# Performance work log

Measured on AMD Instinct MI355X. Metric: run time of the kernel, lower is better.

Reference implementation:

```python
import jax, jax.numpy as jnp
import numpy as np

N_IN, N_OUT, KNN, N_EL = 100000, 25000, 9, 200000
B, C_IN, C_OUT = 4, 8, 16


def setup_inputs() -> dict:
    key = jax.random.key(0)
    ks = jax.random.split(key, 16)
    M = N_OUT * KNN
    inp = {
        "features": jax.random.normal(ks[0], (B, C_IN, N_IN), jnp.float32),
        "domain_points": jax.random.uniform(ks[1], (N_IN, 2), jnp.float32),
        "range_points": jax.random.uniform(ks[2], (N_OUT, 2), jnp.float32),
        # kNN structure: each range point i has exactly KNN support edges
        "eval_idx_dst": jnp.repeat(jnp.arange(N_OUT, dtype=jnp.int32), KNN),
        "eval_idx_src": jax.random.randint(ks[3], (M,), 0, N_IN, jnp.int32),
        "element_list": jax.random.randint(ks[4], (N_EL, 3), 0, N_IN, jnp.int32),
        # Siren filter MLP: 2 -> 16 x5 -> C_IN*C_OUT (outermost linear)
        "siren_w_in": jax.random.normal(ks[5], (2, 16), jnp.float32) / jnp.sqrt(2.0),
        "siren_b_in": jax.random.normal(ks[6], (16,), jnp.float32) * 0.1,
        "siren_wh": jax.random.normal(ks[7], (4, 16, 16), jnp.float32) / 4.0,
        "siren_bh": jax.random.normal(ks[8], (4, 16), jnp.float32) * 0.1,
        "siren_w_out": jax.random.normal(ks[9], (16, C_IN * C_OUT), jnp.float32) / 4.0,
        "siren_b_out": jax.random.normal(ks[10], (C_IN * C_OUT,), jnp.float32) * 0.1,
        # weight_map: 6 -> 8 -> 8 -> 8 -> 3, all sigmoid
        "wm_w0": jax.random.normal(ks[11], (6, 8), jnp.float32) / jnp.sqrt(6.0),
        "wm_b0": jnp.zeros((8,), jnp.float32),
        "wm_w1": jax.random.normal(ks[12], (8, 8), jnp.float32) / jnp.sqrt(8.0),
        "wm_b1": jnp.zeros((8,), jnp.float32),
        "wm_w2": jax.random.normal(ks[13], (8, 8), jnp.float32) / jnp.sqrt(8.0),
        "wm_b2": jnp.zeros((8,), jnp.float32),
        "wm_w3": jax.random.normal(ks[14], (8, 3), jnp.float32) / jnp.sqrt(8.0),
        "wm_b3": jnp.zeros((3,), jnp.float32),
    }
    return inp


def reference(features, domain_points, range_points, eval_idx_src, eval_idx_dst,
              element_list, siren_w_in, siren_b_in, siren_wh, siren_bh,
              siren_w_out, siren_b_out, wm_w0, wm_b0, wm_w1, wm_b1,
              wm_w2, wm_b2, wm_w3, wm_b3):
    omega_0 = 1.0
    n_in = domain_points.shape[0]
    n_out = range_points.shape[0]
    c_in = features.shape[1]
    c_out = siren_w_out.shape[1] // c_in

    # --- eval_weight_map: per-element MLP + scatter_add to per-node weights ---
    el_pts = domain_points[element_list].reshape(element_list.shape[0], -1)  # [E, 6]
    h = jax.nn.sigmoid(el_pts @ wm_w0 + wm_b0)
    h = jax.nn.sigmoid(h @ wm_w1 + wm_b1)
    h = jax.nn.sigmoid(h @ wm_w2 + wm_b2)
    el_w = jax.nn.sigmoid(h @ wm_w3 + wm_b3)  # [E, 3]
    node_w = jax.ops.segment_sum(el_w.reshape(-1), element_list.reshape(-1),
                                 num_segments=n_in)  # [N_in]
    w = node_w[eval_idx_src]  # [M]

    # --- per-edge Siren filter on relative locations ---
    locs = range_points[eval_idx_dst] - domain_points[eval_idx_src]  # [M, 2]
    h = jnp.sin(omega_0 * (locs @ siren_w_in + siren_b_in))
    for i in range(siren_wh.shape[0]):  # fixed small layer count
        h = jnp.sin(omega_0 * (h @ siren_wh[i] + siren_bh[i]))
    filt = ((h @ siren_w_out + siren_b_out)
            .reshape(-1, c_in, c_out)) / c_in  # [M, C_in, C_out]

    # --- weighted gather -> contract -> scatter (quadrature integral) ---
    gathered = features[:, :, eval_idx_src]  # [B, C_in, M]
    values = jnp.einsum('n,nij,bin->bjn', w, filt, gathered)  # [B, C_out, M]
    seg = jax.ops.segment_sum(values.transpose(2, 0, 1), eval_idx_dst,
                              num_segments=n_out)  # [N_out, B, C_out]
    return seg.transpose(1, 2, 0)  # [B, C_out, N_out]
```

## Files before the change

### kernel.cpp

```cpp
#include <hip/hip_runtime.h>

#define N_IN   100000
#define N_OUT  25000
#define KNN    9
#define N_EL   200000
#define BB     4
#define C_IN   8
#define C_OUT  16
#define M_EDGE (N_OUT * KNN)

#define DPB  28
#define EPB  (DPB * KNN)
#define SOP  65

__global__ void __launch_bounds__(256) elem_kernel(
    const int*   __restrict__ el,
    const float* __restrict__ dp,
    const float* __restrict__ w0, const float* __restrict__ b0,
    const float* __restrict__ w1, const float* __restrict__ b1,
    const float* __restrict__ w2, const float* __restrict__ b2,
    const float* __restrict__ w3, const float* __restrict__ b3,
    float* __restrict__ node_w)
{
    int e = blockIdx.x * 256 + threadIdx.x;
    if (e >= N_EL) return;
    int i0 = el[e*3+0], i1 = el[e*3+1], i2 = el[e*3+2];
    float2 p0 = ((const float2*)dp)[i0];
    float2 p1 = ((const float2*)dp)[i1];
    float2 p2 = ((const float2*)dp)[i2];
    float p[6] = { p0.x, p0.y, p1.x, p1.y, p2.x, p2.y };

    float h[8], h2[8];
#pragma unroll
    for (int k = 0; k < 8; ++k) {
        float t = b0[k];
#pragma unroll
        for (int j = 0; j < 6; ++j) t = fmaf(p[j], w0[j*8+k], t);
        h[k] = 1.f / (1.f + __expf(-t));
    }
#pragma unroll
    for (int k = 0; k < 8; ++k) {
        float t = b1[k];
#pragma unroll
        for (int j = 0; j < 8; ++j) t = fmaf(h[j], w1[j*8+k], t);
        h2[k] = 1.f / (1.f + __expf(-t));
    }
#pragma unroll
    for (int k = 0; k < 8; ++k) {
        float t = b2[k];
#pragma unroll
        for (int j = 0; j < 8; ++j) t = fmaf(h2[j], w2[j*8+k], t);
        h[k] = 1.f / (1.f + __expf(-t));
    }
    float o[3];
#pragma unroll
    for (int k = 0; k < 3; ++k) {
        float t = b3[k];
#pragma unroll
        for (int j = 0; j < 8; ++j) t = fmaf(h[j], w3[j*3+k], t);
        o[k] = 1.f / (1.f + __expf(-t));
    }
    atomicAdd(&node_w[i0], o[0]);
    atomicAdd(&node_w[i1], o[1]);
    atomicAdd(&node_w[i2], o[2]);
}

__global__ void __launch_bounds__(256) prep_kernel(
    const float* __restrict__ f, float* __restrict__ ft,
    const float* __restrict__ w_out, float* __restrict__ w_out_t,
    float* __restrict__ node_w)
{
    int n = blockIdx.x * 256 + threadIdx.x;
    if (n < C_IN * C_OUT * 16)
        w_out_t[n] = w_out[(n & 15) * 128 + (n >> 4)];
    if (n >= N_IN) return;
    node_w[n] = 0.f;
    float v[32];
#pragma unroll
    for (int c = 0; c < 32; ++c) v[c] = f[c * N_IN + n];
    float4* dst = (float4*)(ft + (size_t)n * 32);
#pragma unroll
    for (int q = 0; q < 8; ++q)
        dst[q] = make_float4(v[q], v[8+q], v[16+q], v[24+q]);
}

template <int FT>
__global__ void __launch_bounds__(256, 4) edge_kernel(
    const float* __restrict__ feat,
    const float* __restrict__ dp,
    const float* __restrict__ rp,
    const int*   __restrict__ src_idx,
    const float* __restrict__ node_w,
    const float* __restrict__ w_in,
    const float* __restrict__ b_in,
    const float* __restrict__ wh,
    const float* __restrict__ bh,
    const float* __restrict__ w_out,
    const float* __restrict__ w_out_t,
    const float* __restrict__ b_out,
    float* __restrict__ out)
{
    __shared__ float s_out[DPB * SOP];
    const int tid = threadIdx.x;

    for (int i = tid; i < DPB * SOP; i += 256) s_out[i] = 0.f;
    __syncthreads();

    const int  e     = blockIdx.x * EPB + tid;
    int        ldst  = tid / KNN;
    const int  dst   = blockIdx.x * DPB + ldst;
    const bool valid = (tid < EPB) && (dst < N_OUT);
    if (!valid) ldst = 0;
    const int  ce    = valid ? e : 0;
    const int  cdst  = valid ? dst : 0;
    const int  src   = src_idx[ce];

    const float wn    = node_w[src];
    const float scale = valid ? wn * 0.125f : 0.f;

    const float2 rpt = ((const float2*)rp)[cdst];
    const float2 dpt = ((const float2*)dp)[src];
    const float lx = rpt.x - dpt.x;
    const float ly = rpt.y - dpt.y;

    float h[16], h2[16];
#pragma unroll
    for (int k = 0; k < 16; ++k)
        h[k] = __sinf(fmaf(lx, w_in[k], fmaf(ly, w_in[16+k], b_in[k])));

#pragma unroll
    for (int L = 0; L < 4; ++L) {
#pragma unroll
        for (int k = 0; k < 16; ++k) h2[k] = bh[L*16 + k];
#pragma unroll
        for (int j = 0; j < 16; ++j) {
            const float hj = h[j];
#pragma unroll
            for (int k = 0; k < 16; ++k)
                h2[k] = fmaf(hj, wh[L*256 + j*16 + k], h2[k]);
        }
#pragma unroll
        for (int k = 0; k < 16; ++k) h[k] = __sinf(h2[k]);
    }

    float acc[BB * 16];
#pragma unroll
    for (int t = 0; t < BB * 16; ++t) acc[t] = 0.f;

    const float4* fp4 = (const float4*)(feat + (size_t)src * 32);
#pragma unroll
    for (int i = 0; i < C_IN; ++i) {
        float4 gb;
        if (FT) {
            gb = fp4[i];
        } else {
            gb = make_float4(feat[(0*8+i) * N_IN + src],
                             feat[(1*8+i) * N_IN + src],
                             feat[(2*8+i) * N_IN + src],
                             feat[(3*8+i) * N_IN + src]);
        }
#pragma unroll
        for (int j = 0; j < 16; ++j) {
            const int col = i*16 + j;
            float f = b_out[col];
#pragma unroll
            for (int k = 0; k < 16; ++k)
                f = fmaf(h[k], FT ? w_out_t[col*16 + k] : w_out[k*128 + col], f);
            f *= scale;
            acc[0*16 + j] = fmaf(f, gb.x, acc[0*16 + j]);
            acc[1*16 + j] = fmaf(f, gb.y, acc[1*16 + j]);
            acc[2*16 + j] = fmaf(f, gb.z, acc[2*16 + j]);
            acc[3*16 + j] = fmaf(f, gb.w, acc[3*16 + j]);
        }
    }

#pragma unroll
    for (int t = 0; t < BB * 16; ++t)
        atomicAdd(&s_out[ldst * SOP + t], acc[t]);
    __syncthreads();

    const int dst0 = blockIdx.x * DPB;
    for (int i = tid; i < DPB * 64; i += 256) {
        const int d = i % DPB;
        const int c = i / DPB;
        const int gdst = dst0 + d;
        if (gdst < N_OUT)
            out[(size_t)c * N_OUT + gdst] = s_out[d * SOP + c];
    }
}

extern "C" void kernel_launch(void* const* d_in, const int* in_sizes, int n_in,
                              void* d_out, int out_size, void* d_ws, size_t ws_size,
                              hipStream_t stream)
{
    (void)in_sizes; (void)n_in; (void)out_size;
    const float* features = (const float*)d_in[0];
    const float* dp       = (const float*)d_in[1];
    const float* rp       = (const float*)d_in[2];
    const int*   src_idx  = (const int*)d_in[4];
    const int*   el       = (const int*)d_in[5];
    const float* w_in     = (const float*)d_in[6];
    const float* b_in     = (const float*)d_in[7];
    const float* wh       = (const float*)d_in[8];
    const float* bh       = (const float*)d_in[9];
    const float* w_out    = (const float*)d_in[10];
    const float* b_out    = (const float*)d_in[11];
    const float* wm_w0    = (const float*)d_in[12];
    const float* wm_b0    = (const float*)d_in[13];
    const float* wm_w1    = (const float*)d_in[14];
    const float* wm_b1    = (const float*)d_in[15];
    const float* wm_w2    = (const float*)d_in[16];
    const float* wm_b2    = (const float*)d_in[17];
    const float* wm_w3    = (const float*)d_in[18];
    const float* wm_b3    = (const float*)d_in[19];
    float* out = (float*)d_out;

    size_t off0 = 0;
    size_t off1 = (off0 + (size_t)N_IN * sizeof(float) + 511) & ~(size_t)511;
    size_t off2 = (off1 + (size_t)N_IN * 32 * sizeof(float) + 511) & ~(size_t)511;
    size_t need = off2 + (size_t)2048 * sizeof(float);
    float* node_w  = (float*)((char*)d_ws + off0);
    float* feat_t  = (float*)((char*)d_ws + off1);
    float* w_out_t = (float*)((char*)d_ws + off2);
    const bool use_t = (ws_size >= need);

    if (use_t) {
        prep_kernel<<<(N_IN + 255) / 256, 256, 0, stream>>>(
            features, feat_t, w_out, w_out_t, node_w);
        elem_kernel<<<(N_EL + 255) / 256, 256, 0, stream>>>(
            el, dp, wm_w0, wm_b0, wm_w1, wm_b1, wm_w2, wm_b2, wm_w3, wm_b3, node_w);
        edge_kernel<1><<<(N_OUT + DPB - 1) / DPB, 256, 0, stream>>>(
            feat_t, dp, rp, src_idx, node_w,
            w_in, b_in, wh, bh, w_out, w_out_t, b_out, out);
    } else {
        hipMemsetAsync(node_w, 0, (size_t)N_IN * sizeof(float), stream);
        elem_kernel<<<(N_EL + 255) / 256, 256, 0, stream>>>(
            el, dp, wm_w0, wm_b0, wm_w1, wm_b1, wm_w2, wm_b2, wm_w3, wm_b3, node_w);
        edge_kernel<0><<<(N_OUT + DPB - 1) / DPB, 256, 0, stream>>>(
            features, dp, rp, src_idx, node_w,
            w_in, b_in, wh, bh, w_out, (const float*)nullptr, b_out, out);
    }
}
```

Measured before the change: 295.7 us.

## Stage MLP weights in LDS, vectorize reads, and chunk output accumulators

Copies the Siren and weight-map MLP weights and biases into shared memory at block start, with the hidden-layer weights pre-transposed so they can be read as float4 vectors. The output projection is split into four column chunks with a non-unrolled outer loop, which cuts live accumulators from 64 to 16 and is meant to ease register pressure under the 4-blocks-per-CU launch bound. The intent is to replace scalar global or constant loads of uniform weights with LDS vector reads. The cost is about 13 KB more LDS per block, which may limit occupancy, plus recomputing the feature loads once per chunk.

```diff
diff --git a/kernel.cpp b/kernel.cpp
--- a/kernel.cpp
+++ b/kernel.cpp
@@ -22,7 +22,20 @@
     const float* __restrict__ w3, const float* __restrict__ b3,
     float* __restrict__ node_w)
 {
-    int e = blockIdx.x * 256 + threadIdx.x;
+    __shared__ float lw0[48], lb0[8], lw1[64], lb1[8], lw2[64], lb2[8],
+                     lw3[24], lb3[3];
+    const int tid = threadIdx.x;
+    if (tid < 48) lw0[tid] = w0[tid];
+    if (tid < 8)  lb0[tid] = b0[tid];
+    if (tid < 64) lw1[tid] = w1[tid];
+    if (tid < 8)  lb1[tid] = b1[tid];
+    if (tid < 64) lw2[tid] = w2[tid];
+    if (tid < 8)  lb2[tid] = b2[tid];
+    if (tid < 24) lw3[tid] = w3[tid];
+    if (tid < 3)  lb3[tid] = b3[tid];
+    __syncthreads();
+
+    int e = blockIdx.x * 256 + tid;
     if (e >= N_EL) return;
     int i0 = el[e*3+0], i1 = el[e*3+1], i2 = el[e*3+2];
     float2 p0 = ((const float2*)dp)[i0];
@@ -33,31 +46,31 @@
     float h[8], h2[8];
 #pragma unroll
     for (int k = 0; k < 8; ++k) {
-        float t = b0[k];
-#pragma unroll
-        for (int j = 0; j < 6; ++j) t = fmaf(p[j], w0[j*8+k], t);
+        float t = lb0[k];
+#pragma unroll
+        for (int j = 0; j < 6; ++j) t = fmaf(p[j], lw0[j*8+k], t);
         h[k] = 1.f / (1.f + __expf(-t));
     }
 #pragma unroll
     for (int k = 0; k < 8; ++k) {
-        float t = b1[k];
-#pragma unroll
-        for (int j = 0; j < 8; ++j) t = fmaf(h[j], w1[j*8+k], t);
+        float t = lb1[k];
+#pragma unroll
+        for (int j = 0; j < 8; ++j) t = fmaf(h[j], lw1[j*8+k], t);
         h2[k] = 1.f / (1.f + __expf(-t));
     }
 #pragma unroll
     for (int k = 0; k < 8; ++k) {
-        float t = b2[k];
-#pragma unroll
-        for (int j = 0; j < 8; ++j) t = fmaf(h2[j], w2[j*8+k], t);
+        float t = lb2[k];
+#pragma unroll
+        for (int j = 0; j < 8; ++j) t = fmaf(h2[j], lw2[j*8+k], t);
         h[k] = 1.f / (1.f + __expf(-t));
     }
     float o[3];
 #pragma unroll
     for (int k = 0; k < 3; ++k) {
-        float t = b3[k];
-#pragma unroll
-        for (int j = 0; j < 8; ++j) t = fmaf(h[j], w3[j*3+k], t);
+        float t = lb3[k];
+#pragma unroll
+        for (int j = 0; j < 8; ++j) t = fmaf(h[j], lw3[j*3+k], t);
         o[k] = 1.f / (1.f + __expf(-t));
     }
     atomicAdd(&node_w[i0], o[0]);
@@ -68,11 +81,14 @@
 __global__ void __launch_bounds__(256) prep_kernel(
     const float* __restrict__ f, float* __restrict__ ft,
     const float* __restrict__ w_out, float* __restrict__ w_out_t,
+    const float* __restrict__ wh, float* __restrict__ wh_t,
     float* __restrict__ node_w)
 {
     int n = blockIdx.x * 256 + threadIdx.x;
     if (n < C_IN * C_OUT * 16)
         w_out_t[n] = w_out[(n & 15) * 128 + (n >> 4)];
+    if (n < 4 * 256)
+        wh_t[n] = wh[(n & ~255) | ((n & 15) * 16) | ((n >> 4) & 15)];
     if (n >= N_IN) return;
     node_w[n] = 0.f;
     float v[32];
@@ -94,6 +110,7 @@
     const float* __restrict__ w_in,
     const float* __restrict__ b_in,
     const float* __restrict__ wh,
+    const float* __restrict__ wh_t,
     const float* __restrict__ bh,
     const float* __restrict__ w_out,
     const float* __restrict__ w_out_t,
@@ -101,8 +118,26 @@
     float* __restrict__ out)
 {
     __shared__ float s_out[DPB * SOP];
+    __shared__ float lw_out[2048];
+    __shared__ float lwh[1024];
+    __shared__ float lb_out[128], lbh[64], lw_in[32], lb_in[16];
     const int tid = threadIdx.x;
 
+    if (FT) {
+        float4* s4 = (float4*)lw_out;
+        const float4* g4 = (const float4*)w_out_t;
+        s4[tid*2]   = g4[tid*2];
+        s4[tid*2+1] = g4[tid*2+1];
+        ((float4*)lwh)[tid & 255] = ((const float4*)wh_t)[tid & 255];
+    } else {
+        for (int i = tid; i < 2048; i += 256) lw_out[i] = w_out[(i & 15) * 128 + (i >> 4)];
+        for (int i = tid; i < 1024; i += 256)
+            lwh[i] = wh[(i & ~255) | ((i & 15) * 16) | ((i >> 4) & 15)];
+    }
+    if (tid < 32) ((float4*)lb_out)[tid] = ((const float4*)b_out)[tid];
+    if (tid < 16) ((float4*)lbh)[tid]   = ((const float4*)bh)[tid];
+    if (tid < 8)  ((float4*)lw_in)[tid] = ((const float4*)w_in)[tid];
+    if (tid < 4)  ((float4*)lb_in)[tid] = ((const float4*)b_in)[tid];
     for (int i = tid; i < DPB * SOP; i += 256) s_out[i] = 0.f;
     __syncthreads();
 
@@ -123,60 +158,77 @@
     const float lx = rpt.x - dpt.x;
     const float ly = rpt.y - dpt.y;
 
-    float h[16], h2[16];
+    float h[16];
 #pragma unroll
     for (int k = 0; k < 16; ++k)
-        h[k] = __sinf(fmaf(lx, w_in[k], fmaf(ly, w_in[16+k], b_in[k])));
+        h[k] = __sinf(fmaf(lx, lw_in[k], fmaf(ly, lw_in[16+k], lb_in[k])));
 
 #pragma unroll
     for (int L = 0; L < 4; ++L) {
-#pragma unroll
-        for (int k = 0; k < 16; ++k) h2[k] = bh[L*16 + k];
-#pragma unroll
-        for (int j = 0; j < 16; ++j) {
-            const float hj = h[j];
-#pragma unroll
-            for (int k = 0; k < 16; ++k)
-                h2[k] = fmaf(hj, wh[L*256 + j*16 + k], h2[k]);
+        float h2[16];
+#pragma unroll
+        for (int k = 0; k < 16; ++k) {
+            float t = lbh[L*16 + k];
+#pragma unroll
+            for (int jq = 0; jq < 4; ++jq) {
+                float4 w = *(const float4*)&lwh[L*256 + k*16 + jq*4];
+                t = fmaf(h[jq*4+0], w.x, t);
+                t = fmaf(h[jq*4+1], w.y, t);
+                t = fmaf(h[jq*4+2], w.z, t);
+                t = fmaf(h[jq*4+3], w.w, t);
+            }
+            h2[k] = t;
         }
 #pragma unroll
         for (int k = 0; k < 16; ++k) h[k] = __sinf(h2[k]);
     }
 
-    float acc[BB * 16];
-#pragma unroll
-    for (int t = 0; t < BB * 16; ++t) acc[t] = 0.f;
-
     const float4* fp4 = (const float4*)(feat + (size_t)src * 32);
-#pragma unroll
-    for (int i = 0; i < C_IN; ++i) {
-        float4 gb;
-        if (FT) {
-            gb = fp4[i];
-        } else {
-            gb = make_float4(feat[(0*8+i) * N_IN + src],
-                             feat[(1*8+i) * N_IN + src],
-                             feat[(2*8+i) * N_IN + src],
-                             feat[(3*8+i) * N_IN + src]);
+#pragma unroll 1
+    for (int jq = 0; jq < 4; ++jq) {
+        float acc[16];
+#pragma unroll
+        for (int t = 0; t < 16; ++t) acc[t] = 0.f;
+#pragma unroll
+        for (int i = 0; i < C_IN; ++i) {
+            float4 gb;
+            if (FT) {
+                gb = fp4[i];
+            } else {
+                gb = make_float4(feat[(0*8+i) * N_IN + src],
+                                 feat[(1*8+i) * N_IN + src],
+                                 feat[(2*8+i) * N_IN + src],
+                                 feat[(3*8+i) * N_IN + src]);
+            }
+#pragma unroll
+            for (int jj = 0; jj < 4; ++jj) {
+                const int col = i*16 + jq*4 + jj;
+                float4 w0 = *(const float4*)&lw_out[col*16 + 0];
+                float4 w1 = *(const float4*)&lw_out[col*16 + 4];
+                float4 w2 = *(const float4*)&lw_out[col*16 + 8];
+                float4 w3 = *(const float4*)&lw_out[col*16 + 12];
+                float f = lb_out[col];
+                f = fmaf(h[0],  w0.x, f); f = fmaf(h[1],  w0.y, f);
+                f = fmaf(h[2],  w0.z, f); f = fmaf(h[3],  w0.w, f);
+                f = fmaf(h[4],  w1.x, f); f = fmaf(h[5],  w1.y, f);
+                f = fmaf(h[6],  w1.z, f); f = fmaf(h[7],  w1.w, f);
+                f = fmaf(h[8],  w2.x, f); f = fmaf(h[9],  w2.y, f);
+                f = fmaf(h[10], w2.z, f); f = fmaf(h[11], w2.w, f);
+                f = fmaf(h[12], w3.x, f); f = fmaf(h[13], w3.y, f);
+                f = fmaf(h[14], w3.z, f); f = fmaf(h[15], w3.w, f);
+                f *= scale;
+                acc[0*4+jj] = fmaf(f, gb.x, acc[0*4+jj]);
+                acc[1*4+jj] = fmaf(f, gb.y, acc[1*4+jj]);
+                acc[2*4+jj] = fmaf(f, gb.z, acc[2*4+jj]);
+                acc[3*4+jj] = fmaf(f, gb.w, acc[3*4+jj]);
+            }
         }
 #pragma unroll
-        for (int j = 0; j < 16; ++j) {
-            const int col = i*16 + j;
-            float f = b_out[col];
-#pragma unroll
-            for (int k = 0; k < 16; ++k)
-                f = fmaf(h[k], FT ? w_out_t[col*16 + k] : w_out[k*128 + col], f);
-            f *= scale;
-            acc[0*16 + j] = fmaf(f, gb.x, acc[0*16 + j]);
-            acc[1*16 + j] = fmaf(f, gb.y, acc[1*16 + j]);
-            acc[2*16 + j] = fmaf(f, gb.z, acc[2*16 + j]);
-            acc[3*16 + j] = fmaf(f, gb.w, acc[3*16 + j]);
-        }
-    }
-
-#pragma unroll
-    for (int t = 0; t < BB * 16; ++t)
-        atomicAdd(&s_out[ldst * SOP + t], acc[t]);
+        for (int b = 0; b < BB; ++b)
+#pragma unroll
+            for (int jj = 0; jj < 4; ++jj)
+                atomicAdd(&s_out[ldst * SOP + b*16 + jq*4 + jj], acc[b*4+jj]);
+    }
     __syncthreads();
 
     const int dst0 = blockIdx.x * DPB;
@@ -218,26 +270,29 @@
     size_t off0 = 0;
     size_t off1 = (off0 + (size_t)N_IN * sizeof(float) + 511) & ~(size_t)511;
     size_t off2 = (off1 + (size_t)N_IN * 32 * sizeof(float) + 511) & ~(size_t)511;
-    size_t need = off2 + (size_t)2048 * sizeof(float);
+    size_t off3 = (off2 + (size_t)2048 * sizeof(float) + 511) & ~(size_t)511;
+    size_t need = off3 + (size_t)1024 * sizeof(float);
     float* node_w  = (float*)((char*)d_ws + off0);
     float* feat_t  = (float*)((char*)d_ws + off1);
     float* w_out_t = (float*)((char*)d_ws + off2);
+    float* wh_t    = (float*)((char*)d_ws + off3);
     const bool use_t = (ws_size >= need);
 
     if (use_t) {
         prep_kernel<<<(N_IN + 255) / 256, 256, 0, stream>>>(
-            features, feat_t, w_out, w_out_t, node_w);
+            features, feat_t, w_out, w_out_t, wh, wh_t, node_w);
         elem_kernel<<<(N_EL + 255) / 256, 256, 0, stream>>>(
             el, dp, wm_w0, wm_b0, wm_w1, wm_b1, wm_w2, wm_b2, wm_w3, wm_b3, node_w);
         edge_kernel<1><<<(N_OUT + DPB - 1) / DPB, 256, 0, stream>>>(
             feat_t, dp, rp, src_idx, node_w,
-            w_in, b_in, wh, bh, w_out, w_out_t, b_out, out);
+            w_in, b_in, wh, wh_t, bh, w_out, w_out_t, b_out, out);
     } else {
         hipMemsetAsync(node_w, 0, (size_t)N_IN * sizeof(float), stream);
         elem_kernel<<<(N_EL + 255) / 256, 256, 0, stream>>>(
             el, dp, wm_w0, wm_b0, wm_w1, wm_b1, wm_w2, wm_b2, wm_w3, wm_b3, node_w);
         edge_kernel<0><<<(N_OUT + DPB - 1) / DPB, 256, 0, stream>>>(
             features, dp, rp, src_idx, node_w,
-            w_in, b_in, wh, bh, w_out, (const float*)nullptr, b_out, out);
-    }
-}
+            w_in, b_in, wh, (const float*)nullptr, bh, w_out,
+            (const float*)nullptr, b_out, out);
+    }
+}
```

Result: faster. 289.2 us (-2.2%).

## Split edge work across threads via LDS-staged Siren hidden states

Applied to the files above, without the earlier changes.

The edge kernel is restructured so that 126 threads per block compute the Siren hidden layers for 14 destinations and stage the results in shared memory. All 256 threads then process (edge, quarter of output columns) pairs, each holding 16 accumulators instead of 64. This cuts register pressure so the launch bound can rise from 4 to 6 blocks per SIMD. The cost is that half the threads sit idle during the MLP phase, plus extra LDS traffic and a second sync, with twice as many blocks overall.

```diff
diff --git a/kernel.cpp b/kernel.cpp
--- a/kernel.cpp
+++ b/kernel.cpp
@@ -7,11 +7,11 @@
 #define BB     4
 #define C_IN   8
 #define C_OUT  16
-#define M_EDGE (N_OUT * KNN)
-
-#define DPB  28
+
+#define DPB  14
 #define EPB  (DPB * KNN)
 #define SOP  65
+#define HST  17
 
 __global__ void __launch_bounds__(256) elem_kernel(
     const int*   __restrict__ el,
@@ -85,7 +85,7 @@
 }
 
 template <int FT>
-__global__ void __launch_bounds__(256, 4) edge_kernel(
+__global__ void __launch_bounds__(256, 6) edge_kernel(
     const float* __restrict__ feat,
     const float* __restrict__ dp,
     const float* __restrict__ rp,
@@ -101,85 +101,109 @@
     float* __restrict__ out)
 {
     __shared__ float s_out[DPB * SOP];
+    __shared__ float h_lds[EPB * HST];
+    __shared__ int   s_src[EPB];
+    __shared__ float s_scale[EPB];
     const int tid = threadIdx.x;
 
     for (int i = tid; i < DPB * SOP; i += 256) s_out[i] = 0.f;
+
+    if (tid < EPB) {
+        const int eg   = blockIdx.x * EPB + tid;
+        const int ldst = tid / KNN;
+        const int dst  = blockIdx.x * DPB + ldst;
+        const bool valid = (dst < N_OUT);
+        const int ce   = valid ? eg : 0;
+        const int src  = src_idx[ce];
+        s_src[tid]   = src;
+        const float wn = node_w[src];
+        s_scale[tid] = valid ? wn * 0.125f : 0.f;
+
+        const float2 rpt = ((const float2*)rp)[valid ? dst : 0];
+        const float2 dpt = ((const float2*)dp)[src];
+        const float lx = rpt.x - dpt.x;
+        const float ly = rpt.y - dpt.y;
+
+        float h[16];
+#pragma unroll
+        for (int k = 0; k < 16; ++k)
+            h[k] = __sinf(fmaf(lx, w_in[k], fmaf(ly, w_in[16+k], b_in[k])));
+
+#pragma unroll
+        for (int L = 0; L < 4; ++L) {
+            float h2[16];
+#pragma unroll
+            for (int k = 0; k < 16; ++k) {
+                float t = bh[L*16 + k];
+#pragma unroll
+                for (int j = 0; j < 16; ++j)
+                    t = fmaf(h[j], wh[L*256 + j*16 + k], t);
+                h2[k] = t;
+            }
+#pragma unroll
+            for (int k = 0; k < 16; ++k) h[k] = __sinf(h2[k]);
+        }
+#pragma unroll
+        for (int k = 0; k < 16; ++k) h_lds[tid * HST + k] = h[k];
+    }
     __syncthreads();
 
-    const int  e     = blockIdx.x * EPB + tid;
-    int        ldst  = tid / KNN;
-    const int  dst   = blockIdx.x * DPB + ldst;
-    const bool valid = (tid < EPB) && (dst < N_OUT);
-    if (!valid) ldst = 0;
-    const int  ce    = valid ? e : 0;
-    const int  cdst  = valid ? dst : 0;
-    const int  src   = src_idx[ce];
-
-    const float wn    = node_w[src];
-    const float scale = valid ? wn * 0.125f : 0.f;
-
-    const float2 rpt = ((const float2*)rp)[cdst];
-    const float2 dpt = ((const float2*)dp)[src];
-    const float lx = rpt.x - dpt.x;
-    const float ly = rpt.y - dpt.y;
-
-    float h[16], h2[16];
-#pragma unroll
-    for (int k = 0; k < 16; ++k)
-        h[k] = __sinf(fmaf(lx, w_in[k], fmaf(ly, w_in[16+k], b_in[k])));
-
-#pragma unroll
-    for (int L = 0; L < 4; ++L) {
-#pragma unroll
-        for (int k = 0; k < 16; ++k) h2[k] = bh[L*16 + k];
-#pragma unroll
-        for (int j = 0; j < 16; ++j) {
-            const float hj = h[j];
-#pragma unroll
-            for (int k = 0; k < 16; ++k)
-                h2[k] = fmaf(hj, wh[L*256 + j*16 + k], h2[k]);
+#pragma unroll 1
+    for (int r = 0; r < 2; ++r) {
+        const int item = tid + r * 256;
+        const int e    = item & 127;
+        const int jq   = __builtin_amdgcn_readfirstlane(item >> 7);
+        if (e < EPB) {
+            const int   src   = s_src[e];
+            const float scale = s_scale[e];
+            float hh[16];
+#pragma unroll
+            for (int k = 0; k < 16; ++k) hh[k] = h_lds[e * HST + k];
+
+            const float4* fp4 = (const float4*)(feat + (size_t)src * 32);
+            float acc[16];
+#pragma unroll
+            for (int t = 0; t < 16; ++t) acc[t] = 0.f;
+#pragma unroll
+            for (int i = 0; i < C_IN; ++i) {
+                float4 gb;
+                if (FT) {
+                    gb = fp4[i];
+                } else {
+                    gb = make_float4(feat[(0*8+i) * N_IN + src],
+                                     feat[(1*8+i) * N_IN + src],
+                                     feat[(2*8+i) * N_IN + src],
+                                     feat[(3*8+i) * N_IN + src]);
+                }
+#pragma unroll
+                for (int jj = 0; jj < 4; ++jj) {
+                    const int col = i*16 + jq*4 + jj;
+                    float f = b_out[col];
+#pragma unroll
+                    for (int k = 0; k < 16; ++k)
+                        f = fmaf(hh[k],
+                                 FT ? w_out_t[col*16 + k] : w_out[k*128 + col],
+                                 f);
+                    f *= scale;
+                    acc[0*4+jj] = fmaf(f, gb.x, acc[0*4+jj]);
+                    acc[1*4+jj] = fmaf(f, gb.y, acc[1*4+jj]);
+                    acc[2*4+jj] = fmaf(f, gb.z, acc[2*4+jj]);
+                    acc[3*4+jj] = fmaf(f, gb.w, acc[3*4+jj]);
+                }
+            }
+            const int ldst = e / KNN;
+#pragma unroll
+            for (int b = 0; b < BB; ++b)
+#pragma unroll
+                for (int jj = 0; jj < 4; ++jj)
+                    atomicAdd(&s_out[ldst * SOP + b*16 + jq*4 + jj],
+                              acc[b*4+jj]);
         }
-#pragma unroll
-        for (int k = 0; k < 16; ++k) h[k] = __sinf(h2[k]);
-    }
-
-    float acc[BB * 16];
-#pragma unroll
-    for (int t = 0; t < BB * 16; ++t) acc[t] = 0.f;
-
-    const float4* fp4 = (const float4*)(feat + (size_t)src * 32);
-#pragma unroll
-    for (int i = 0; i < C_IN; ++i) {
-        float4 gb;
-        if (FT) {
-            gb = fp4[i];
-        } else {
-            gb = make_float4(feat[(0*8+i) * N_IN + src],
-                             feat[(1*8+i) * N_IN + src],
-                             feat[(2*8+i) * N_IN + src],
-                             feat[(3*8+i) * N_IN + src]);
-        }
-#pragma unroll
-        for (int j = 0; j < 16; ++j) {
-            const int col = i*16 + j;
-            float f = b_out[col];
-#pragma unroll
-            for (int k = 0; k < 16; ++k)
-                f = fmaf(h[k], FT ? w_out_t[col*16 + k] : w_out[k*128 + col], f);
-            f *= scale;
-            acc[0*16 + j] = fmaf(f, gb.x, acc[0*16 + j]);
-            acc[1*16 + j] = fmaf(f, gb.y, acc[1*16 + j]);
-            acc[2*16 + j] = fmaf(f, gb.z, acc[2*16 + j]);
-            acc[3*16 + j] = fmaf(f, gb.w, acc[3*16 + j]);
-        }
-    }
-
-#pragma unroll
-    for (int t = 0; t < BB * 16; ++t)
-        atomicAdd(&s_out[ldst * SOP + t], acc[t]);
+    }
     __syncthreads();
 
     const int dst0 = blockIdx.x * DPB;
+#pragma unroll 1
     for (int i = tid; i < DPB * 64; i += 256) {
         const int d = i % DPB;
         const int c = i / DPB;
@@ -224,19 +248,21 @@
     float* w_out_t = (float*)((char*)d_ws + off2);
     const bool use_t = (ws_size >= need);
 
+    const int edge_blocks = (N_OUT + DPB - 1) / DPB;
+
     if (use_t) {
         prep_kernel<<<(N_IN + 255) / 256, 256, 0, stream>>>(
             features, feat_t, w_out, w_out_t, node_w);
         elem_kernel<<<(N_EL + 255) / 256, 256, 0, stream>>>(
             el, dp, wm_w0, wm_b0, wm_w1, wm_b1, wm_w2, wm_b2, wm_w3, wm_b3, node_w);
-        edge_kernel<1><<<(N_OUT + DPB - 1) / DPB, 256, 0, stream>>>(
+        edge_kernel<1><<<edge_blocks, 256, 0, stream>>>(
             feat_t, dp, rp, src_idx, node_w,
             w_in, b_in, wh, bh, w_out, w_out_t, b_out, out);
     } else {
         hipMemsetAsync(node_w, 0, (size_t)N_IN * sizeof(float), stream);
         elem_kernel<<<(N_EL + 255) / 256, 256, 0, stream>>>(
             el, dp, wm_w0, wm_b0, wm_w1, wm_b1, wm_w2, wm_b2, wm_w3, wm_b3, node_w);
-        edge_kernel<0><<<(N_OUT + DPB - 1) / DPB, 256, 0, stream>>>(
+        edge_kernel<0><<<edge_blocks, 256, 0, stream>>>(
             features, dp, rp, src_idx, node_w,
             w_in, b_in, wh, bh, w_out, (const float*)nullptr, b_out, out);
     }
```

Result: faster. 260.4 us (-11.9%).
